# Kernel optimization log

Measured on AMD Instinct MI355X. Metric: run time of the kernel, lower is better.

## Reference

```python
import jax, jax.numpy as jnp
import numpy as np

B, T, ENC_IN, DEC_IN, U = 32768, 7, 60, 36, 356


def setup_inputs() -> dict:
    key = jax.random.key(0)
    ks = jax.random.split(key, 12)
    s = 0.05  # small weight scale for numerical sanity
    return {
        "x_batch": jax.random.normal(ks[0], (B, T, ENC_IN), jnp.float32),
        "m_batch": jax.random.normal(ks[1], (B, T, DEC_IN), jnp.float32),
        "enc_kernel": jax.random.normal(ks[2], (ENC_IN, 4 * U), jnp.float32) * s,
        "enc_rec_kernel": jax.random.normal(ks[3], (U, 4 * U), jnp.float32) * s,
        "enc_bias": jnp.zeros((4 * U,), jnp.float32),
        "dec_kernel": jax.random.normal(ks[4], (DEC_IN, 4 * U), jnp.float32) * s,
        "dec_rec_kernel": jax.random.normal(ks[5], (U, 4 * U), jnp.float32) * s,
        "dec_bias": jnp.zeros((4 * U,), jnp.float32),
        "W_map": jax.random.normal(ks[6], (T * U, 768), jnp.float32) * s,
        "b_map": jnp.zeros((768,), jnp.float32),
        "W_deep1": jax.random.normal(ks[7], (768, 768), jnp.float32) * s,
        "b_deep1": jnp.zeros((768,), jnp.float32),
        "W_deep2": jax.random.normal(ks[8], (768, 768), jnp.float32) * s,
        "b_deep2": jnp.zeros((768,), jnp.float32),
        "W_out": jax.random.normal(ks[9], (768, 168), jnp.float32) * s,
        "b_out": jnp.zeros((168,), jnp.float32),
    }


def _lstm(x, K, R, b, h0, c0):
    """Keras-style LSTM. x: [B,T,D]. Returns (hs [B,T,U], h_T, c_T).
    Gate order i, f, g(candidate), o; sigmoid recurrent activation, tanh activation."""
    xz = jnp.einsum('btd,dg->btg', x, K) + b  # precompute input projections [B,T,4U]

    def step(carry, xz_t):
        h, c = carry
        z = xz_t + h @ R
        i, f, g, o = jnp.split(z, 4, axis=-1)
        c = jax.nn.sigmoid(f) * c + jax.nn.sigmoid(i) * jnp.tanh(g)
        h = jax.nn.sigmoid(o) * jnp.tanh(c)
        return (h, c), h

    (h, c), hs = jax.lax.scan(step, (h0, c0), jnp.swapaxes(xz, 0, 1))
    return jnp.swapaxes(hs, 0, 1), h, c


def reference(x_batch, m_batch, enc_kernel, enc_rec_kernel, enc_bias,
              dec_kernel, dec_rec_kernel, dec_bias,
              W_map, b_map, W_deep1, b_deep1, W_deep2, b_deep2, W_out, b_out):
    b = x_batch.shape[0]
    z = jnp.zeros((b, U), x_batch.dtype)
    # encoder: only final states used
    _, s_h, s_c = _lstm(x_batch, enc_kernel, enc_rec_kernel, enc_bias, z, z)
    # decoder: full sequence, initialized with encoder states
    decoded, _, _ = _lstm(m_batch, dec_kernel, dec_rec_kernel, dec_bias, s_h, s_c)
    f = decoded.reshape(b, -1)  # [B, 7*356]
    m = jax.nn.relu(f @ W_map + b_map)
    d = jnp.tanh(m @ W_deep1 + b_deep1)
    d = jnp.tanh(d @ W_deep2 + b_deep2)
    return d @ W_out + b_out
```

## Files before the change

### kernel.cpp

```cpp
#include <hip/hip_runtime.h>

typedef unsigned short u16;
typedef __attribute__((ext_vector_type(8))) short short8;
typedef __attribute__((ext_vector_type(4))) float f32x4;

#define B_ROWS 32768
#define T_STEPS 7
#define ENC_INd 60
#define DEC_INd 36
#define UNITS 356
#define KP_LSTM 448
#define H_OFF 64
#define HID 768
#define OUTN 168
#define OUTNP 256
#define KMAP 2688
#define HALF_E 44040192ull
#define WLSTM_E 688128
#define CG_BLK 6144

__device__ __forceinline__ u16 f2b(float f) {
  unsigned u = __builtin_bit_cast(unsigned, f);
  u += 0x7fffu + ((u >> 16) & 1u);
  return (u16)(u >> 16);
}
__device__ __forceinline__ float sigm(float x) { return 1.0f / (1.0f + __expf(-x)); }
__device__ __forceinline__ float tanhfast(float x) { return 2.0f / (1.0f + __expf(-2.0f * x)) - 1.0f; }

__device__ __forceinline__ void stage16(const u16* g, u16* l) {
  __builtin_amdgcn_global_load_lds((const __attribute__((address_space(1))) void*)g,
                                   (__attribute__((address_space(3))) void*)l, 16, 0, 0);
}

__global__ void fill_sentinel(float* __restrict__ out, int n, float v) {
  int i = blockIdx.x * 256 + threadIdx.x;
  int stride = gridDim.x * 256;
  for (; i < n; i += stride) out[i] = v;
}

__global__ void prep_lstm_w(const float* __restrict__ Km, const float* __restrict__ Rm,
                            const float* __restrict__ bias, int in_dim,
                            u16* __restrict__ WT, float* __restrict__ bias_r)
{
  int idx = blockIdx.x * 256 + threadIdx.x;
  if (idx >= WLSTM_E) return;
  int e    = idx & 7;
  int lane = (idx >> 3) & 63;
  int nf   = (idx >> 9) & 3;
  int t1   = idx >> 11;
  int kk   = t1 % 14;
  int g    = t1 / 14;
  int u = g * 16 + (lane & 15);
  int k = kk * 32 + ((lane >> 4) << 3) + e;
  float v = 0.f;
  if (u < UNITS) {
    int oc = nf * UNITS + u;
    if (k < in_dim) v = Km[(size_t)k * 1424 + oc];
    else if (k >= H_OFF && k < H_OFF + UNITS) v = Rm[(size_t)(k - H_OFF) * 1424 + oc];
    if (k == 0) bias_r[(u << 2) + nf] = bias[oc];
  } else if (k == 0) bias_r[(u << 2) + nf] = 0.f;
  WT[idx] = f2b(v);
}

__global__ void prep_map_w(const float* __restrict__ W, u16* __restrict__ WT)
{
  int idx = blockIdx.x * 256 + threadIdx.x;
  if (idx >= HID * KMAP) return;
  int n = idx / KMAP, k = idx - n * KMAP;
  int t = k / 384, kk = k - t * 384;
  float v = (kk < UNITS) ? W[(size_t)(t * UNITS + kk) * HID + n] : 0.f;
  WT[idx] = f2b(v);
}

__global__ void prep_mlp_w(const float* __restrict__ W, int korig, int norig, int kp,
                           u16* __restrict__ WT, int total)
{
  int idx = blockIdx.x * 256 + threadIdx.x;
  if (idx >= total) return;
  int n = idx / kp, k = idx - n * kp;
  float v = (k < korig && n < norig) ? W[(size_t)k * norig + n] : 0.f;
  WT[idx] = f2b(v);
}

__global__ __launch_bounds__(512)
void lstm_persistent(const float* __restrict__ xg, const float* __restrict__ mg,
                     const u16* __restrict__ WTe, const float* __restrict__ bre,
                     const u16* __restrict__ WTd, const float* __restrict__ brd,
                     u16* __restrict__ fbuf,
                     f32x4* __restrict__ cg0, f32x4* __restrict__ cg1, f32x4* __restrict__ cg2)
{
  __shared__ __align__(16) u16 A[2][64][KP_LSTM];

  const int tid = threadIdx.x;
  const int ns = tid >> 6;
  const int lane = tid & 63;
  const int l15 = lane & 15, l4 = lane >> 4;
  const int blk = blockIdx.x;
  const int row0 = blk * 64;

  f32x4* cgb;
  if (blk < 224)      cgb = cg0 + (size_t)blk * CG_BLK;
  else if (blk < 480) cgb = cg1 + (size_t)(blk - 224) * CG_BLK;
  else                cgb = cg2 + (size_t)(blk - 480) * CG_BLK;

  {
    short8 z = {};
    for (int q = tid; q < 6144; q += 512) {
      int buf = q / 3072, rem = q - buf * 3072;
      int row = rem / 48, blkc = 8 + (rem - row * 48);
      *(short8*)&A[buf][row][blkc << 3] = z;
    }
  }

#pragma unroll 1
  for (int s = 0; s < 14; ++s) {
    const u16*  wt = (s < 7) ? WTe : WTd;
    const float* br = (s < 7) ? bre : brd;
    const float* src = (s < 7) ? xg : mg;
    const int in_dim = (s < 7) ? ENC_INd : DEC_INd;
    const int t = (s < 7) ? s : s - 7;
    const int par = s & 1;

    {
      const int row = tid >> 3, cb = tid & 7;
      const float* sp = src + ((size_t)(row0 + row) * T_STEPS + t) * in_dim;
      const int cbs = cb ^ (row & 7);
      short8 vv;
#pragma unroll
      for (int j = 0; j < 8; ++j) {
        const int cc = (cb << 3) + j;
        float v = (cc < in_dim) ? sp[cc] : 0.f;
        vv[j] = (short)f2b(v);
      }
      *(short8*)&A[par][row][cbs << 3] = vv;
    }
    __syncthreads();

#pragma unroll 1
    for (int p = 0; p < 3; ++p) {
      const int g = p * 8 + ns;
      f32x4 acc[4][4] = {};
      const u16* bp = wt + ((size_t)g * 14) * 2048 + (lane << 3);

      f32x4 cw0, cw1, cw2, cw3;
      if (s > 0) {
        const int cib = (p * 4) * 512 + tid;
        cw0 = cgb[cib];
        cw1 = cgb[cib + 512];
        cw2 = cgb[cib + 1024];
        cw3 = cgb[cib + 1536];
      } else {
        cw0 = f32x4{0.f, 0.f, 0.f, 0.f}; cw1 = cw0; cw2 = cw0; cw3 = cw0;
      }

#pragma unroll 1
      for (int kk = 0; kk < 14; ++kk) {
        short8 bf[4];
#pragma unroll
        for (int nf = 0; nf < 4; ++nf)
          bf[nf] = *(const short8*)(bp + kk * 2048 + (nf << 9));
        const int cbA = (kk << 2) + l4;
        {
          short8 af0[2];
#pragma unroll
          for (int mf = 0; mf < 2; ++mf) {
            const int ra = (mf << 4) + l15;
            const int cbs = (cbA & 56) | ((cbA ^ ra) & 7);
            af0[mf] = *(const short8*)&A[par][ra][cbs << 3];
          }
#pragma unroll
          for (int mf = 0; mf < 2; ++mf)
#pragma unroll
            for (int nf = 0; nf < 4; ++nf)
              acc[mf][nf] = __builtin_amdgcn_mfma_f32_16x16x32_bf16(af0[mf], bf[nf], acc[mf][nf], 0, 0, 0);
        }
        {
          short8 af1[2];
#pragma unroll
          for (int mf = 0; mf < 2; ++mf) {
            const int ra = ((mf + 2) << 4) + l15;
            const int cbs = (cbA & 56) | ((cbA ^ ra) & 7);
            af1[mf] = *(const short8*)&A[par][ra][cbs << 3];
          }
#pragma unroll
          for (int mf = 0; mf < 2; ++mf)
#pragma unroll
            for (int nf = 0; nf < 4; ++nf)
              acc[mf + 2][nf] = __builtin_amdgcn_mfma_f32_16x16x32_bf16(af1[mf], bf[nf], acc[mf + 2][nf], 0, 0, 0);
        }
      }

      const int u = (g << 4) + l15;
      const int ch = H_OFF + u, cbh = ch >> 3, cih = ch & 7;
      float bz[4];
#pragma unroll
      for (int nf = 0; nf < 4; ++nf) bz[nf] = br[(u << 2) + nf];
#pragma unroll
      for (int mf = 0; mf < 4; ++mf) {
        f32x4 cw = (mf == 0) ? cw0 : (mf == 1) ? cw1 : (mf == 2) ? cw2 : cw3;
#pragma unroll
        for (int r = 0; r < 4; ++r) {
          const int row = (mf << 4) + (l4 << 2) + r;
          float zi = acc[mf][0][r] + bz[0];
          float zf = acc[mf][1][r] + bz[1];
          float zg = acc[mf][2][r] + bz[2];
          float zo = acc[mf][3][r] + bz[3];
          float ig = sigm(zi), fg = sigm(zf);
          float gg = tanhfast(zg), og = sigm(zo);
          float cn = fg * cw[r] + ig * gg;
          cw[r] = cn;
          float hv = og * tanhfast(cn);
          u16 hb = f2b(hv);
          const int cbs = (cbh & 56) | ((cbh ^ row) & 7);
          A[par ^ 1][row][(cbs << 3) + cih] = hb;
          if (s >= 7) {
            const int grow = row0 + row;
            __builtin_nontemporal_store(hb,
              &fbuf[(size_t)(grow >> 14) * HALF_E
                    + ((size_t)(grow & 16383) * T_STEPS + t) * 384 + u]);
          }
        }
        cgb[(p * 4 + mf) * 512 + tid] = cw;
      }
    }
  }
}

template<int MODE>
__global__ __launch_bounds__(256)
void mlp_gemm(const u16* __restrict__ A, int lda, int kp,
              const u16* __restrict__ WT, const float* __restrict__ bias, int nreal,
              u16* __restrict__ outb, float* __restrict__ outf, int ldo)
{
  __shared__ __align__(16) u16 lds_a[128 * 64];
  __shared__ __align__(16) u16 lds_b[128 * 64];
  const int tid = threadIdx.x;
  const int wid = tid >> 6, lane = tid & 63;
  const int wm = (wid >> 1) << 6, wn = (wid & 1) << 6;
  const int l15 = lane & 15, l4 = lane >> 4;
  const size_t abase = (size_t)blockIdx.x * 128 * lda;
  const size_t bbase = (size_t)blockIdx.y * 128 * kp;

  f32x4 acc[4][4] = {};

  for (int kt = 0; kt < kp; kt += 64) {
#pragma unroll
    for (int q = 0; q < 4; ++q) {
      const int u = q * 256 + tid;
      const int r = u >> 3, cb = u & 7;
      const int cs = kt + ((cb ^ (r & 7)) << 3);
      u16* da = &lds_a[(q * 256 + (wid << 6)) * 8];
      u16* db = &lds_b[(q * 256 + (wid << 6)) * 8];
      stage16(A + abase + (size_t)r * lda + cs, da);
      stage16(WT + bbase + (size_t)r * kp + cs, db);
    }
    __syncthreads();
#pragma unroll
    for (int kk = 0; kk < 2; ++kk) {
      short8 af[4], bfr[4];
#pragma unroll
      for (int mf = 0; mf < 4; ++mf) {
        int ra = wm + (mf << 4) + l15;
        int cb = (kk << 2) + l4;
        af[mf] = *(const short8*)&lds_a[(ra << 6) + ((cb ^ (ra & 7)) << 3)];
      }
#pragma unroll
      for (int nf = 0; nf < 4; ++nf) {
        int rb = wn + (nf << 4) + l15;
        int cb = (kk << 2) + l4;
        bfr[nf] = *(const short8*)&lds_b[(rb << 6) + ((cb ^ (rb & 7)) << 3)];
      }
#pragma unroll
      for (int mf = 0; mf < 4; ++mf)
#pragma unroll
        for (int nf = 0; nf < 4; ++nf)
          acc[mf][nf] = __builtin_amdgcn_mfma_f32_16x16x32_bf16(af[mf], bfr[nf], acc[mf][nf], 0, 0, 0);
    }
    __syncthreads();
  }

#pragma unroll
  for (int mf = 0; mf < 4; ++mf) {
    int rowb = blockIdx.x * 128 + wm + (mf << 4) + (l4 << 2);
#pragma unroll
    for (int r = 0; r < 4; ++r) {
      int row = rowb + r;
#pragma unroll
      for (int nf = 0; nf < 4; ++nf) {
        int n = blockIdx.y * 128 + wn + (nf << 4) + l15;
        float v = acc[mf][nf][r];
        size_t oi = (size_t)row * ldo + n;
        if (MODE == 3) {
          outb[oi] = f2b(tanhfast(v + bias[n]));
        } else if (MODE == 5) {
          outb[oi] = f2b(fmaxf(v + bias[n], 0.f));
        } else {
          if (n < nreal) outf[oi] = v + bias[n];
        }
      }
    }
  }
}

extern "C" void kernel_launch(void* const* d_in, const int* in_sizes, int n_in,
                              void* d_out, int out_size, void* d_ws, size_t ws_size,
                              hipStream_t stream)
{
  const float* x    = (const float*)d_in[0];
  const float* m    = (const float*)d_in[1];
  const float* ek   = (const float*)d_in[2];
  const float* erk  = (const float*)d_in[3];
  const float* eb   = (const float*)d_in[4];
  const float* dk   = (const float*)d_in[5];
  const float* drk  = (const float*)d_in[6];
  const float* dbi  = (const float*)d_in[7];
  const float* wmap = (const float*)d_in[8];
  const float* bmap = (const float*)d_in[9];
  const float* wd1  = (const float*)d_in[10];
  const float* bd1  = (const float*)d_in[11];
  const float* wd2  = (const float*)d_in[12];
  const float* bd2  = (const float*)d_in[13];
  const float* wout = (const float*)d_in[14];
  const float* bout = (const float*)d_in[15];

  char* ws = (char*)d_ws;
  size_t off = 0;
  auto alloc = [&](size_t bytes) { char* p = ws + off; off += (bytes + 255) & ~(size_t)255; return p; };

  u16*   WT_enc  = (u16*)  alloc((size_t)WLSTM_E * 2);
  u16*   WT_dec  = (u16*)  alloc((size_t)WLSTM_E * 2);
  float* b_enc_r = (float*)alloc((size_t)384 * 4 * 4);
  float* b_dec_r = (float*)alloc((size_t)384 * 4 * 4);
  u16*   WT_map  = (u16*)  alloc((size_t)HID * KMAP * 2);
  u16*   WT_d1   = (u16*)  alloc((size_t)HID * HID * 2);
  u16*   WT_d2   = (u16*)  alloc((size_t)HID * HID * 2);
  u16*   WT_out  = (u16*)  alloc((size_t)OUTNP * HID * 2);
  u16*   m1_h1   = (u16*)  alloc((size_t)16384 * HID * 2);
  u16*   fbuf    = (u16*)  alloc((size_t)2 * HALF_E * 2);
  f32x4* cg2     = (f32x4*)alloc((size_t)32 * CG_BLK * 16);
  const size_t NEED = off;

  if (ws_size < NEED) {
    fill_sentinel<<<256, 256, 0, stream>>>((float*)d_out, out_size, (float)(ws_size >> 20));
    return;
  }

  f32x4* cg0 = (f32x4*)d_out;
  f32x4* cg1 = (f32x4*)m1_h1;

  u16* fb_h0 = fbuf;
  u16* fb_h1 = fbuf + HALF_E;
  u16* m1_h0 = fb_h1;
  u16* m2_h0 = fb_h0;
  u16* m2_h1 = fb_h0 + (size_t)16384 * HID;
  u16* m3_h0 = fb_h1;
  u16* m3_h1 = m1_h1;

  prep_lstm_w<<<(WLSTM_E + 255) / 256, 256, 0, stream>>>(ek, erk, eb, ENC_INd, WT_enc, b_enc_r);
  prep_lstm_w<<<(WLSTM_E + 255) / 256, 256, 0, stream>>>(dk, drk, dbi, DEC_INd, WT_dec, b_dec_r);
  prep_map_w<<<((HID * KMAP) + 255) / 256, 256, 0, stream>>>(wmap, WT_map);
  prep_mlp_w<<<((HID * HID) + 255) / 256, 256, 0, stream>>>(wd1, HID, HID, HID, WT_d1, HID * HID);
  prep_mlp_w<<<((HID * HID) + 255) / 256, 256, 0, stream>>>(wd2, HID, HID, HID, WT_d2, HID * HID);
  prep_mlp_w<<<((OUTNP * HID) + 255) / 256, 256, 0, stream>>>(wout, HID, OUTN, HID, WT_out, OUTNP * HID);

  lstm_persistent<<<512, 512, 0, stream>>>(x, m, WT_enc, b_enc_r, WT_dec, b_dec_r, fbuf,
                                           cg0, cg1, cg2);

  mlp_gemm<5><<<dim3(128, 6), 256, 0, stream>>>(fb_h1, KMAP, KMAP, WT_map, bmap, HID, m1_h1, nullptr, HID);
  mlp_gemm<5><<<dim3(128, 6), 256, 0, stream>>>(fb_h0, KMAP, KMAP, WT_map, bmap, HID, m1_h0, nullptr, HID);
  mlp_gemm<3><<<dim3(128, 6), 256, 0, stream>>>(m1_h0, HID, HID, WT_d1, bd1, HID, m2_h0, nullptr, HID);
  mlp_gemm<3><<<dim3(128, 6), 256, 0, stream>>>(m1_h1, HID, HID, WT_d1, bd1, HID, m2_h1, nullptr, HID);
  mlp_gemm<3><<<dim3(128, 6), 256, 0, stream>>>(m2_h0, HID, HID, WT_d2, bd2, HID, m3_h0, nullptr, HID);
  mlp_gemm<3><<<dim3(128, 6), 256, 0, stream>>>(m2_h1, HID, HID, WT_d2, bd2, HID, m3_h1, nullptr, HID);
  mlp_gemm<4><<<dim3(128, 2), 256, 0, stream>>>(m3_h0, HID, HID, WT_out, bout, OUTN,
                                                nullptr, (float*)d_out, OUTN);
  mlp_gemm<4><<<dim3(128, 2), 256, 0, stream>>>(m3_h1, HID, HID, WT_out, bout, OUTN,
                                                nullptr, (float*)d_out + (size_t)16384 * OUTN, OUTN);
}
```

Baseline: 1.460 ms.

## Switch LSTM recurrent GEMM to 32x32x16 MFMA with repartitioned wave tiling

```diff
diff --git a/kernel.cpp b/kernel.cpp
--- a/kernel.cpp
+++ b/kernel.cpp
@@ -3,6 +3,7 @@
 typedef unsigned short u16;
 typedef __attribute__((ext_vector_type(8))) short short8;
 typedef __attribute__((ext_vector_type(4))) float f32x4;
+typedef __attribute__((ext_vector_type(16))) float f32x16;
 
 #define B_ROWS 32768
 #define T_STEPS 7
@@ -48,10 +49,10 @@
   int lane = (idx >> 3) & 63;
   int nf   = (idx >> 9) & 3;
   int t1   = idx >> 11;
-  int kk   = t1 % 14;
-  int g    = t1 / 14;
-  int u = g * 16 + (lane & 15);
-  int k = kk * 32 + ((lane >> 4) << 3) + e;
+  int ks   = t1 % 28;
+  int g32  = t1 / 28;
+  int u = g32 * 32 + (lane & 31);
+  int k = ks * 16 + ((lane >> 5) << 3) + e;
   float v = 0.f;
   if (u < UNITS) {
     int oc = nf * UNITS + u;
@@ -92,9 +93,11 @@
   __shared__ __align__(16) u16 A[2][64][KP_LSTM];
 
   const int tid = threadIdx.x;
-  const int ns = tid >> 6;
+  const int ns = (tid >> 6) & 3;
+  const int mh = tid >> 8;
   const int lane = tid & 63;
-  const int l15 = lane & 15, l4 = lane >> 4;
+  const int l31 = lane & 31, lh = lane >> 5;
+  const int frow = mh * 32 + l31;
   const int blk = blockIdx.x;
   const int row0 = blk * 64;
 
@@ -102,6 +105,11 @@
   if (blk < 224)      cgb = cg0 + (size_t)blk * CG_BLK;
   else if (blk < 480) cgb = cg1 + (size_t)(blk - 224) * CG_BLK;
   else                cgb = cg2 + (size_t)(blk - 480) * CG_BLK;
+
+  int offm[4];
+#pragma unroll
+  for (int m = 0; m < 4; ++m)
+    offm[m] = frow * 896 + ((((m << 1) + lh) ^ frow) & 7) * 16;
 
   {
     short8 z = {};
@@ -136,11 +144,13 @@
     }
     __syncthreads();
 
+    const char* Abase = (const char*)&A[par][0][0];
+
 #pragma unroll 1
     for (int p = 0; p < 3; ++p) {
-      const int g = p * 8 + ns;
-      f32x4 acc[4][4] = {};
-      const u16* bp = wt + ((size_t)g * 14) * 2048 + (lane << 3);
+      const int g32 = p * 4 + ns;
+      f32x16 acc[4] = {};
+      const char* bp = (const char*)(wt + (size_t)g32 * 28 * 4 * 512 + (lane << 3));
 
       f32x4 cw0, cw1, cw2, cw3;
       if (s > 0) {
@@ -153,74 +163,51 @@
         cw0 = f32x4{0.f, 0.f, 0.f, 0.f}; cw1 = cw0; cw2 = cw0; cw3 = cw0;
       }
 
-#pragma unroll 1
-      for (int kk = 0; kk < 14; ++kk) {
-        short8 bf[4];
-#pragma unroll
-        for (int nf = 0; nf < 4; ++nf)
-          bf[nf] = *(const short8*)(bp + kk * 2048 + (nf << 9));
-        const int cbA = (kk << 2) + l4;
-        {
-          short8 af0[2];
-#pragma unroll
-          for (int mf = 0; mf < 2; ++mf) {
-            const int ra = (mf << 4) + l15;
-            const int cbs = (cbA & 56) | ((cbA ^ ra) & 7);
-            af0[mf] = *(const short8*)&A[par][ra][cbs << 3];
-          }
-#pragma unroll
-          for (int mf = 0; mf < 2; ++mf)
-#pragma unroll
-            for (int nf = 0; nf < 4; ++nf)
-              acc[mf][nf] = __builtin_amdgcn_mfma_f32_16x16x32_bf16(af0[mf], bf[nf], acc[mf][nf], 0, 0, 0);
-        }
-        {
-          short8 af1[2];
-#pragma unroll
-          for (int mf = 0; mf < 2; ++mf) {
-            const int ra = ((mf + 2) << 4) + l15;
-            const int cbs = (cbA & 56) | ((cbA ^ ra) & 7);
-            af1[mf] = *(const short8*)&A[par][ra][cbs << 3];
-          }
-#pragma unroll
-          for (int mf = 0; mf < 2; ++mf)
-#pragma unroll
-            for (int nf = 0; nf < 4; ++nf)
-              acc[mf + 2][nf] = __builtin_amdgcn_mfma_f32_16x16x32_bf16(af1[mf], bf[nf], acc[mf + 2][nf], 0, 0, 0);
-        }
-      }
-
-      const int u = (g << 4) + l15;
+#pragma unroll
+      for (int ks = 0; ks < 28; ++ks) {
+        short8 af = *(const short8*)(Abase + offm[ks & 3] + ((ks >> 2) << 7));
+        short8 b0 = *(const short8*)(bp + ks * 4096);
+        short8 b1 = *(const short8*)(bp + ks * 4096 + 1024);
+        short8 b2 = *(const short8*)(bp + ks * 4096 + 2048);
+        short8 b3 = *(const short8*)(bp + ks * 4096 + 3072);
+        acc[0] = __builtin_amdgcn_mfma_f32_32x32x16_bf16(af, b0, acc[0], 0, 0, 0);
+        acc[1] = __builtin_amdgcn_mfma_f32_32x32x16_bf16(af, b1, acc[1], 0, 0, 0);
+        acc[2] = __builtin_amdgcn_mfma_f32_32x32x16_bf16(af, b2, acc[2], 0, 0, 0);
+        acc[3] = __builtin_amdgcn_mfma_f32_32x32x16_bf16(af, b3, acc[3], 0, 0, 0);
+      }
+
+      const int u = g32 * 32 + l31;
       const int ch = H_OFF + u, cbh = ch >> 3, cih = ch & 7;
       float bz[4];
 #pragma unroll
       for (int nf = 0; nf < 4; ++nf) bz[nf] = br[(u << 2) + nf];
 #pragma unroll
-      for (int mf = 0; mf < 4; ++mf) {
-        f32x4 cw = (mf == 0) ? cw0 : (mf == 1) ? cw1 : (mf == 2) ? cw2 : cw3;
-#pragma unroll
-        for (int r = 0; r < 4; ++r) {
-          const int row = (mf << 4) + (l4 << 2) + r;
-          float zi = acc[mf][0][r] + bz[0];
-          float zf = acc[mf][1][r] + bz[1];
-          float zg = acc[mf][2][r] + bz[2];
-          float zo = acc[mf][3][r] + bz[3];
+      for (int q = 0; q < 4; ++q) {
+        f32x4 cw = (q == 0) ? cw0 : (q == 1) ? cw1 : (q == 2) ? cw2 : cw3;
+#pragma unroll
+        for (int rr = 0; rr < 4; ++rr) {
+          const int r = q * 4 + rr;
+          const int orow = mh * 32 + rr + (q << 3) + (lh << 2);
+          float zi = acc[0][r] + bz[0];
+          float zf = acc[1][r] + bz[1];
+          float zg = acc[2][r] + bz[2];
+          float zo = acc[3][r] + bz[3];
           float ig = sigm(zi), fg = sigm(zf);
           float gg = tanhfast(zg), og = sigm(zo);
-          float cn = fg * cw[r] + ig * gg;
-          cw[r] = cn;
+          float cn = fg * cw[rr] + ig * gg;
+          cw[rr] = cn;
           float hv = og * tanhfast(cn);
           u16 hb = f2b(hv);
-          const int cbs = (cbh & 56) | ((cbh ^ row) & 7);
-          A[par ^ 1][row][(cbs << 3) + cih] = hb;
+          const int cbs = (cbh & 56) | ((cbh ^ orow) & 7);
+          A[par ^ 1][orow][(cbs << 3) + cih] = hb;
           if (s >= 7) {
-            const int grow = row0 + row;
+            const int grow = row0 + orow;
             __builtin_nontemporal_store(hb,
               &fbuf[(size_t)(grow >> 14) * HALF_E
                     + ((size_t)(grow & 16383) * T_STEPS + t) * 384 + u]);
           }
         }
-        cgb[(p * 4 + mf) * 512 + tid] = cw;
+        cgb[(p * 4 + q) * 512 + tid] = cw;
       }
     }
   }
```

After: 3.261 ms. 2.23x slower.

## Halve LSTM block to 4 waves and prefetch recurrent weights four k-steps ahead

Applied to the files above, without the earlier changes.

```diff
diff --git a/kernel.cpp b/kernel.cpp
--- a/kernel.cpp
+++ b/kernel.cpp
@@ -82,7 +82,7 @@
   WT[idx] = f2b(v);
 }
 
-__global__ __launch_bounds__(512)
+__global__ __launch_bounds__(256)
 void lstm_persistent(const float* __restrict__ xg, const float* __restrict__ mg,
                      const u16* __restrict__ WTe, const float* __restrict__ bre,
                      const u16* __restrict__ WTd, const float* __restrict__ brd,
@@ -105,7 +105,7 @@
 
   {
     short8 z = {};
-    for (int q = tid; q < 6144; q += 512) {
+    for (int q = tid; q < 6144; q += 256) {
       int buf = q / 3072, rem = q - buf * 3072;
       int row = rem / 48, blkc = 8 + (rem - row * 48);
       *(short8*)&A[buf][row][blkc << 3] = z;
@@ -122,72 +122,69 @@
     const int par = s & 1;
 
     {
-      const int row = tid >> 3, cb = tid & 7;
+      const int row = tid >> 2;
       const float* sp = src + ((size_t)(row0 + row) * T_STEPS + t) * in_dim;
-      const int cbs = cb ^ (row & 7);
-      short8 vv;
-#pragma unroll
-      for (int j = 0; j < 8; ++j) {
-        const int cc = (cb << 3) + j;
-        float v = (cc < in_dim) ? sp[cc] : 0.f;
-        vv[j] = (short)f2b(v);
-      }
-      *(short8*)&A[par][row][cbs << 3] = vv;
+#pragma unroll
+      for (int qq = 0; qq < 2; ++qq) {
+        const int cb = ((tid & 3) << 1) + qq;
+        const int cbs = cb ^ (row & 7);
+        short8 vv;
+#pragma unroll
+        for (int j = 0; j < 8; ++j) {
+          const int cc = (cb << 3) + j;
+          float v = (cc < in_dim) ? sp[cc] : 0.f;
+          vv[j] = (short)f2b(v);
+        }
+        *(short8*)&A[par][row][cbs << 3] = vv;
+      }
     }
     __syncthreads();
 
 #pragma unroll 1
-    for (int p = 0; p < 3; ++p) {
-      const int g = p * 8 + ns;
+    for (int p = 0; p < 6; ++p) {
+      const int g = p * 4 + ns;
       f32x4 acc[4][4] = {};
       const u16* bp = wt + ((size_t)g * 14) * 2048 + (lane << 3);
 
       f32x4 cw0, cw1, cw2, cw3;
       if (s > 0) {
-        const int cib = (p * 4) * 512 + tid;
+        const int cib = (p * 4) * 256 + tid;
         cw0 = cgb[cib];
-        cw1 = cgb[cib + 512];
-        cw2 = cgb[cib + 1024];
-        cw3 = cgb[cib + 1536];
+        cw1 = cgb[cib + 256];
+        cw2 = cgb[cib + 512];
+        cw3 = cgb[cib + 768];
       } else {
         cw0 = f32x4{0.f, 0.f, 0.f, 0.f}; cw1 = cw0; cw2 = cw0; cw3 = cw0;
       }
 
-#pragma unroll 1
+      short8 b0[4], b1[4], b2[4], b3[4];
+      auto LOADB = [&](short8* d, int kk) {
+#pragma unroll
+        for (int nf = 0; nf < 4; ++nf)
+          d[nf] = *(const short8*)(bp + kk * 2048 + (nf << 9));
+      };
+      auto MSTEP = [&](int kk, short8* b) {
+        const int cbA = (kk << 2) + l4;
+        short8 af[4];
+#pragma unroll
+        for (int mf = 0; mf < 4; ++mf) {
+          const int ra = (mf << 4) + l15;
+          const int cbs = (cbA & 56) | ((cbA ^ ra) & 7);
+          af[mf] = *(const short8*)&A[par][ra][cbs << 3];
+        }
+#pragma unroll
+        for (int mf = 0; mf < 4; ++mf)
+#pragma unroll
+          for (int nf = 0; nf < 4; ++nf)
+            acc[mf][nf] = __builtin_amdgcn_mfma_f32_16x16x32_bf16(af[mf], b[nf], acc[mf][nf], 0, 0, 0);
+      };
+
+      LOADB(b0, 0); LOADB(b1, 1); LOADB(b2, 2); LOADB(b3, 3);
+#pragma unroll
       for (int kk = 0; kk < 14; ++kk) {
-        short8 bf[4];
-#pragma unroll
-        for (int nf = 0; nf < 4; ++nf)
-          bf[nf] = *(const short8*)(bp + kk * 2048 + (nf << 9));
-        const int cbA = (kk << 2) + l4;
-        {
-          short8 af0[2];
-#pragma unroll
-          for (int mf = 0; mf < 2; ++mf) {
-            const int ra = (mf << 4) + l15;
-            const int cbs = (cbA & 56) | ((cbA ^ ra) & 7);
-            af0[mf] = *(const short8*)&A[par][ra][cbs << 3];
-          }
-#pragma unroll
-          for (int mf = 0; mf < 2; ++mf)
-#pragma unroll
-            for (int nf = 0; nf < 4; ++nf)
-              acc[mf][nf] = __builtin_amdgcn_mfma_f32_16x16x32_bf16(af0[mf], bf[nf], acc[mf][nf], 0, 0, 0);
-        }
-        {
-          short8 af1[2];
-#pragma unroll
-          for (int mf = 0; mf < 2; ++mf) {
-            const int ra = ((mf + 2) << 4) + l15;
-            const int cbs = (cbA & 56) | ((cbA ^ ra) & 7);
-            af1[mf] = *(const short8*)&A[par][ra][cbs << 3];
-          }
-#pragma unroll
-          for (int mf = 0; mf < 2; ++mf)
-#pragma unroll
-            for (int nf = 0; nf < 4; ++nf)
-              acc[mf + 2][nf] = __builtin_amdgcn_mfma_f32_16x16x32_bf16(af1[mf], bf[nf], acc[mf + 2][nf], 0, 0, 0);
-        }
+        short8* bc = ((kk & 3) == 0) ? b0 : ((kk & 3) == 1) ? b1 : ((kk & 3) == 2) ? b2 : b3;
+        MSTEP(kk, bc);
+        if (kk + 4 < 14) LOADB(bc, kk + 4);
       }
 
       const int u = (g << 4) + l15;
@@ -220,7 +217,7 @@
                     + ((size_t)(grow & 16383) * T_STEPS + t) * 384 + u]);
           }
         }
-        cgb[(p * 4 + mf) * 512 + tid] = cw;
+        cgb[(p * 4 + mf) * 256 + tid] = cw;
       }
     }
   }
@@ -363,7 +360,7 @@
   prep_mlp_w<<<((HID * HID) + 255) / 256, 256, 0, stream>>>(wd2, HID, HID, HID, WT_d2, HID * HID);
   prep_mlp_w<<<((OUTNP * HID) + 255) / 256, 256, 0, stream>>>(wout, HID, OUTN, HID, WT_out, OUTNP * HID);
 
-  lstm_persistent<<<512, 512, 0, stream>>>(x, m, WT_enc, b_enc_r, WT_dec, b_dec_r, fbuf,
+  lstm_persistent<<<512, 256, 0, stream>>>(x, m, WT_enc, b_enc_r, WT_dec, b_dec_r, fbuf,
                                            cg0, cg1, cg2);
 
   mlp_gemm<5><<<dim3(128, 6), 256, 0, stream>>>(fb_h1, KMAP, KMAP, WT_map, bmap, HID, m1_h1, nullptr, HID);
```

Result: slower. 2.000 ms (+37.0%).
